# Kernel tuning notes

Measured on AMD Instinct MI355X. Metric: run time of the kernel, lower is better.

## Reference

```python
import jax, jax.numpy as jnp
import numpy as np
from jax import lax

# ---- module config (init_kwargs) ----
B, CIN, COUT, H, W, K = 16, 32, 32, 256, 256, 3
FEATURE_BITS = 8
INPUT_ZP = 3
OUTPUT_ZP = -5
INPUT_SCALE = 0.02
OUTPUT_SCALE = 0.05
STRIDE = (1, 1)
PAD_H, PAD_W = 1, 1
DILATION = (1, 1)
GROUPS = 1
QMIN, QMAX = -(2 ** (FEATURE_BITS - 1)), 2 ** (FEATURE_BITS - 1) - 1  # -128, 127


def float_to_fixed_point(scale, bitwidth):
    # Represent scale (in (0,1)) as int_scale * 2^-frac_bits with int_scale <= 2^(b-1)-1.
    # Pick the largest frac_bits s.t. round(scale * 2^frac_bits) fits -> max precision.
    qmax = jnp.float32(2 ** (bitwidth - 1) - 1)
    frac_bits = jnp.floor(jnp.log2(qmax / scale)).astype(jnp.int32)
    int_scale = jnp.round(scale * jnp.exp2(frac_bits.astype(jnp.float32))).astype(jnp.int32)
    return int_scale, frac_bits


def setup_inputs() -> dict:
    key = jax.random.key(0)
    k0, k1, k2, k3 = jax.random.split(key, 4)
    x = jax.random.randint(k0, (B, CIN, H, W), -128, 128, dtype=jnp.int32).astype(jnp.int8)
    qweight = jax.random.randint(k1, (COUT, CIN, K, K), -128, 128, dtype=jnp.int32).astype(jnp.int8)
    qbias = jax.random.randint(k2, (COUT,), -1000, 1000, dtype=jnp.int32)
    weight_scale = jax.random.uniform(k3, (COUT,), jnp.float32, 1e-3, 1e-2)
    return {"x": x, "qweight": qweight, "qbias": qbias, "weight_scale": weight_scale}


def reference(x, qweight, qbias, weight_scale):
    # F.pad(qinput, (pw,pw,ph,ph), 'constant', input_zero_point) -> pad W and H dims
    xp = jnp.pad(x, ((0, 0), (0, 0), (PAD_H, PAD_H), (PAD_W, PAD_W)),
                 mode="constant", constant_values=INPUT_ZP)
    # int32 conv (no bias), VALID since input was pre-padded
    out = lax.conv_general_dilated(
        xp.astype(jnp.int32), qweight.astype(jnp.int32),
        window_strides=STRIDE, padding="VALID", rhs_dilation=DILATION,
        dimension_numbers=("NCHW", "OIHW", "NCHW"), feature_group_count=GROUPS)
    # shifted bias: qbias - sum(qweight) * input_zero_point  (per out channel)
    shifted_qbias = qbias - qweight.astype(jnp.int32).sum((1, 2, 3)) * INPUT_ZP
    out = out + shifted_qbias[None, :, None, None]
    # fixed-point requant: (out * int_scale) >> frac_bits, per channel
    folded_scale = (INPUT_SCALE * weight_scale / OUTPUT_SCALE).astype(jnp.float32)
    int_scale, frac_bits = float_to_fixed_point(folded_scale, FEATURE_BITS)
    out = jnp.right_shift(out * int_scale[None, :, None, None],
                          frac_bits[None, :, None, None])  # arithmetic shift on int32
    out = out + OUTPUT_ZP
    out = jnp.clip(out, QMIN, QMAX).astype(jnp.int8)
    return out
```

## Files before the change

kernel.cpp:

```cpp
#include <hip/hip_runtime.h>

#define B_   16
#define CIN  32
#define COUT 32
#define H_   256
#define W_   256
#define IN_ZP  3
#define OUT_ZP (-5)
#define HW (H_ * W_)
#define TH 8
#define TW 64
#define SW 72
#define SH 10

#define XPH 258
#define XPW 264
#define XPQ 66
#define PLANE_W (XPH * XPW)
#define XP_WORDS (B_ * 8 * PLANE_W)
#define WS_TAB 2400
#define WS_NEED ((size_t)(WS_TAB + XP_WORDS) * 4)
#define NQ (B_ * 8 * XPH * XPQ)
#define PACK_BLOCKS 2176


using i32x4  = __attribute__((ext_vector_type(4))) int;
using i32x16 = __attribute__((ext_vector_type(16))) int;


__global__ __launch_bounds__(256) void qconv_pack(const int* __restrict__ x,
                                                  const int* __restrict__ qw,
                                                  const int* __restrict__ qb,
                                                  const float* __restrict__ wscale,
                                                  int* __restrict__ ws) {
    const int bid = blockIdx.x;
    const int tid = threadIdx.x;
    if (bid < 32) {
        __shared__ int red[4];
        const int co = bid;
        const int* wco = qw + co * (CIN * 9);
        int s = 0;
        for (int i = tid; i < CIN * 9; i += 256) s += wco[i];
        for (int off = 32; off; off >>= 1) s += __shfl_down(s, off, 64);
        if ((tid & 63) == 0) red[tid >> 6] = s;

        if (tid < 72) {
            int gidx = co * 72 + tid;
            int g    = gidx & 3;
            int lane = (gidx >> 2) & 63;
            int t    = gidx >> 8;
            int wco2 = lane & 31;
            int ci0  = 16 * (lane >> 5) + 4 * g;
            const int* base = qw + wco2 * (CIN * 9);
            int b0 = base[(ci0 + 0) * 9 + t] & 0xff;
            int b1 = base[(ci0 + 1) * 9 + t] & 0xff;
            int b2 = base[(ci0 + 2) * 9 + t] & 0xff;
            int b3 = base[(ci0 + 3) * 9 + t] & 0xff;
            ws[gidx] = b0 | (b1 << 8) | (b2 << 16) | (b3 << 24);
        }
        __syncthreads();
        if (tid == 0) {
            int wsum = red[0] + red[1] + red[2] + red[3];
            ws[2304 + co] = qb[co] - wsum * IN_ZP;
            float fs = (0.02f * wscale[co]) / 0.05f;
            float fb = floorf(log2f(127.0f / fs));
            int isc = (int)rintf(fs * exp2f(fb));
            ws[2336 + co] = isc | (((int)fb) << 16);
        }
        return;
    }
    int* __restrict__ xp = ws + WS_TAB;
    const int T = (PACK_BLOCKS) * 256;
    for (int q = (bid - 32) * 256 + tid; q < NQ; q += T) {
        int b   = q / (8 * XPH * XPQ);
        int r1  = q - b * (8 * XPH * XPQ);
        int cig = r1 / (XPH * XPQ);
        int r2  = r1 - cig * (XPH * XPQ);
        int ph  = r2 / XPQ;
        int cq  = r2 - ph * XPQ;
        int gh  = ph - 1;
        int gw0 = cq * 4 - 4;
        int ghc = min(H_ - 1, max(0, gh));
        int gwc = min(W_ - 4, max(0, gw0));
        const int* p = x + (b * CIN + cig * 4) * HW + ghc * W_ + gwc;
        i32x4 v0 = *(const i32x4*)(p);
        i32x4 v1 = *(const i32x4*)(p + HW);
        i32x4 v2 = *(const i32x4*)(p + 2 * HW);
        i32x4 v3 = *(const i32x4*)(p + 3 * HW);
        bool vh = (unsigned)gh < (unsigned)H_;
        i32x4 pk;
#pragma unroll
        for (int j = 0; j < 4; ++j) {
            int t = (v0[j] & 0xff) | ((v1[j] & 0xff) << 8) |
                    ((v2[j] & 0xff) << 16) | (v3[j] << 24);
            bool ok = vh && ((unsigned)(gw0 + j) < (unsigned)W_);
            pk[j] = ok ? t : 0x03030303;
        }
        *(i32x4*)(xp + 4 * q) = pk;
    }
}

#define SMEM(cig_, r_, c_) sl[((cig_) * SH + (r_)) * SW + (c_)]
__global__ __launch_bounds__(256) void qconv_fused(const int* __restrict__ ws,
                                                   int* __restrict__ out) {
    __shared__ __align__(16) int sl[6144];
    __shared__ __align__(16) int cons[64];

    const int d  = blockIdx.x + 4 * blockIdx.y + 128 * blockIdx.z;
    const int w  = ((d & 7) << 8) | (d >> 3);
    const int tx = w & 3;
    const int ty = (w >> 2) & 31;
    const int tb = w >> 7;

    const int wt = tx * TW;
    const int ht = ty * TH;
    const int tid = threadIdx.x;
    const int lane = tid & 63, wv = tid >> 6;
    const int* __restrict__ xp = ws + WS_TAB;

    if (tid < 64) cons[tid] = ws[2304 + tid];

    const int rowbase = (tb * 8) * XPH + ht;
#pragma unroll
    for (int k = 0; k < 6; ++k) {
        int idx = 256 * k + 64 * wv + lane;
        idx = min(idx, 1439);
        int cig = idx / 180;
        int rem = idx - cig * 180;
        const int* src = xp + (rowbase + cig * XPH + rem / 18) * XPW
                            + wt + 4 * (rem - (rem / 18) * 18);
        __builtin_amdgcn_global_load_lds(
            (const __attribute__((address_space(1))) void*)src,
            (__attribute__((address_space(3))) void*)(sl + 4 * (256 * k + 64 * wv)),
            16, 0, 0);
    }

    i32x4 wfrag[9];
    const i32x4* wsv = (const i32x4*)ws;
#pragma unroll
    for (int t = 0; t < 9; ++t) wfrag[t] = wsv[t * 64 + lane];

    __syncthreads();

    const int hh  = lane >> 5;
    const int pix = lane & 31;

#pragma unroll
    for (int i = 0; i < 4; ++i) {
        const int mt = wv * 4 + i;
        const int r0 = mt >> 1, chunk = mt & 1;
        i32x16 acc;
#pragma unroll
        for (int r = 0; r < 16; ++r) acc[r] = 0;
#pragma unroll
        for (int t = 0; t < 9; ++t) {
            const int dh = t / 3, dw = t % 3;
            const int rr = r0 + dh;
            const int c  = chunk * 32 + pix + dw + 3;
            i32x4 a;
#pragma unroll
            for (int g = 0; g < 4; ++g) a[g] = SMEM(4 * hh + g, rr, c);
            acc = __builtin_amdgcn_mfma_i32_32x32x32_i8(wfrag[t], a, acc, 0, 0, 0);
        }
        int* op = out + (tb * COUT) * HW + (ht + r0) * W_ + wt + chunk * 32 + pix;
#pragma unroll
        for (int rg = 0; rg < 4; ++rg) {
            const int cb = 4 * hh + 8 * rg;
            i32x4 sb4 = *(const i32x4*)&cons[cb];
            i32x4 qf4 = *(const i32x4*)&cons[32 + cb];
#pragma unroll
            for (int j = 0; j < 4; ++j) {
                int q = qf4[j];
                int v = acc[rg * 4 + j] + sb4[j];
                v = (int)((unsigned)v * (unsigned)(q & 0xffff)) >> (q >> 16);
                v += OUT_ZP;
                v = min(127, max(-128, v));
                op[(cb + j) * HW] = v;
            }
        }
    }
}
#undef SMEM

__global__ void qconv_prep_fb(const int* __restrict__ qw, const int* __restrict__ qb,
                              const float* __restrict__ wscale, int* __restrict__ ws) {
    const int co  = blockIdx.x;
    const int tid = threadIdx.x;
    __shared__ int red[4];
    const int* wco = qw + co * (CIN * 9);
    int s = 0;
    for (int i = tid; i < CIN * 9; i += 256) s += wco[i];
    for (int off = 32; off; off >>= 1) s += __shfl_down(s, off, 64);
    if ((tid & 63) == 0) red[tid >> 6] = s;
    if (tid < 72) {
        int gidx = blockIdx.x * 72 + tid;
        int g    = gidx & 3;
        int lane = (gidx >> 2) & 63;
        int t    = gidx >> 8;
        int wco2 = lane & 31;
        int ci0  = 16 * (lane >> 5) + 4 * g;
        const int* base = qw + wco2 * (CIN * 9);
        int b0 = base[(ci0 + 0) * 9 + t] & 0xff;
        int b1 = base[(ci0 + 1) * 9 + t] & 0xff;
        int b2 = base[(ci0 + 2) * 9 + t] & 0xff;
        int b3 = base[(ci0 + 3) * 9 + t] & 0xff;
        ws[gidx] = b0 | (b1 << 8) | (b2 << 16) | (b3 << 24);
    }
    __syncthreads();
    if (tid == 0) {
        int wsum = red[0] + red[1] + red[2] + red[3];
        ws[2304 + co] = qb[co] - wsum * IN_ZP;
        float fs = (0.02f * wscale[co]) / 0.05f;
        float fb = floorf(log2f(127.0f / fs));
        int isc = (int)rintf(fs * exp2f(fb));
        ws[2336 + co] = isc | (((int)fb) << 16);
    }
}

__device__ __forceinline__ void stage_item(int idx, int ht, int wt,
                                           const int* __restrict__ xb,
                                           int (*smem)[SH][SW]) {
    int cig = idx / 180;
    int rem = idx - cig * 180;
    int r   = rem / 18;
    int c4  = rem - r * 18;
    int gh  = ht - 1 + r;
    int gw0 = wt - 4 + c4 * 4;
    int ghc = min(H_ - 1, max(0, gh));
    int gwc = min(W_ - 4, max(0, gw0));
    const int* p = xb + (cig * 4) * HW + ghc * W_ + gwc;
    i32x4 v0 = *(const i32x4*)(p);
    i32x4 v1 = *(const i32x4*)(p + HW);
    i32x4 v2 = *(const i32x4*)(p + 2 * HW);
    i32x4 v3 = *(const i32x4*)(p + 3 * HW);
    bool vh = (unsigned)gh < (unsigned)H_;
    i32x4 pk;
#pragma unroll
    for (int j = 0; j < 4; ++j) {
        int t = (v0[j] & 0xff) | ((v1[j] & 0xff) << 8) |
                ((v2[j] & 0xff) << 16) | (v3[j] << 24);
        bool ok = vh && ((unsigned)(gw0 + j) < (unsigned)W_);
        pk[j] = ok ? t : 0x03030303;
    }
    *(i32x4*)&smem[cig][r][c4 * 4] = pk;
}

__global__ __launch_bounds__(256) void qconv_fused_fb(const int* __restrict__ x,
                                                      const int* __restrict__ ws,
                                                      int* __restrict__ out) {
    __shared__ int smem[8][SH][SW];
    __shared__ __align__(16) int cons[64];
    const int d  = blockIdx.x + 4 * blockIdx.y + 128 * blockIdx.z;
    const int w  = ((d & 7) << 8) | (d >> 3);
    const int tx = w & 3;
    const int ty = (w >> 2) & 31;
    const int tb = w >> 7;
    const int wt = tx * TW;
    const int ht = ty * TH;
    const int tid = threadIdx.x;
    const int* xb = x + tb * (CIN * HW);
    if (tid < 64) cons[tid] = ws[2304 + tid];
    stage_item(tid,        ht, wt, xb, smem);
    stage_item(tid + 256,  ht, wt, xb, smem);
    stage_item(tid + 512,  ht, wt, xb, smem);
    stage_item(tid + 768,  ht, wt, xb, smem);
    stage_item(tid + 1024, ht, wt, xb, smem);
    if (tid < 160) stage_item(tid + 1280, ht, wt, xb, smem);
    __syncthreads();
    const int lane = tid & 63, wv = tid >> 6;
    const int hh  = lane >> 5;
    const int pix = lane & 31;
    i32x4 wfrag[9];
    const i32x4* wsv = (const i32x4*)ws;
#pragma unroll
    for (int t = 0; t < 9; ++t) wfrag[t] = wsv[t * 64 + lane];
#pragma unroll
    for (int i = 0; i < 4; ++i) {
        const int mt = wv * 4 + i;
        const int r0 = mt >> 1, chunk = mt & 1;
        i32x16 acc;
#pragma unroll
        for (int r = 0; r < 16; ++r) acc[r] = 0;
#pragma unroll
        for (int t = 0; t < 9; ++t) {
            const int dh = t / 3, dw = t % 3;
            const int rr = r0 + dh;
            const int c  = chunk * 32 + pix + dw + 3;
            i32x4 a;
#pragma unroll
            for (int g = 0; g < 4; ++g) a[g] = smem[4 * hh + g][rr][c];
            acc = __builtin_amdgcn_mfma_i32_32x32x32_i8(wfrag[t], a, acc, 0, 0, 0);
        }
        int* op = out + (tb * COUT) * HW + (ht + r0) * W_ + wt + chunk * 32 + pix;
#pragma unroll
        for (int rg = 0; rg < 4; ++rg) {
            const int cb = 4 * hh + 8 * rg;
            i32x4 sb4 = *(const i32x4*)&cons[cb];
            i32x4 qf4 = *(const i32x4*)&cons[32 + cb];
#pragma unroll
            for (int j = 0; j < 4; ++j) {
                int q = qf4[j];
                int v = acc[rg * 4 + j] + sb4[j];
                v = (int)((unsigned)v * (unsigned)(q & 0xffff)) >> (q >> 16);
                v += OUT_ZP;
                v = min(127, max(-128, v));
                op[(cb + j) * HW] = v;
            }
        }
    }
}

extern "C" void kernel_launch(void* const* d_in, const int* in_sizes, int n_in,
                              void* d_out, int out_size, void* d_ws, size_t ws_size,
                              hipStream_t stream) {
    const int*   x   = (const int*)d_in[0];
    const int*   qw  = (const int*)d_in[1];
    const int*   qb  = (const int*)d_in[2];
    const float* wsc = (const float*)d_in[3];
    int* ws  = (int*)d_ws;
    int* out = (int*)d_out;
    dim3 grid(W_ / TW, H_ / TH, B_);

    if (ws_size >= WS_NEED) {
        qconv_pack<<<32 + PACK_BLOCKS, 256, 0, stream>>>(x, qw, qb, wsc, ws);
        qconv_fused<<<grid, 256, 0, stream>>>(ws, out);
    } else {
        qconv_prep_fb<<<32, 256, 0, stream>>>(qw, qb, wsc, ws);
        qconv_fused_fb<<<grid, 256, 0, stream>>>(x, ws, out);
    }
}
```

Baseline: 251.1 us.

## Read packed input directly from global memory instead of LDS staging

Removes the shared-memory tile and its global_load_lds staging, so each lane loads the MFMA A operands straight from the packed padded input in global memory, relying on L1/L2 for reuse across the nine taps. The tile loop is no longer unrolled and output stores become nontemporal. This drops the LDS round trip and its latency, but every tap now issues scalar global loads, which adds memory traffic and exposes latency that is no longer hidden behind a single barrier.

```diff
diff --git a/kernel.cpp b/kernel.cpp
--- a/kernel.cpp
+++ b/kernel.cpp
@@ -100,10 +100,8 @@
     }
 }
 
-#define SMEM(cig_, r_, c_) sl[((cig_) * SH + (r_)) * SW + (c_)]
 __global__ __launch_bounds__(256) void qconv_fused(const int* __restrict__ ws,
                                                    int* __restrict__ out) {
-    __shared__ __align__(16) int sl[6144];
     __shared__ __align__(16) int cons[64];
 
     const int d  = blockIdx.x + 4 * blockIdx.y + 128 * blockIdx.z;
@@ -116,24 +114,11 @@
     const int ht = ty * TH;
     const int tid = threadIdx.x;
     const int lane = tid & 63, wv = tid >> 6;
+    const int hh  = lane >> 5;
+    const int pix = lane & 31;
     const int* __restrict__ xp = ws + WS_TAB;
 
     if (tid < 64) cons[tid] = ws[2304 + tid];
-
-    const int rowbase = (tb * 8) * XPH + ht;
-#pragma unroll
-    for (int k = 0; k < 6; ++k) {
-        int idx = 256 * k + 64 * wv + lane;
-        idx = min(idx, 1439);
-        int cig = idx / 180;
-        int rem = idx - cig * 180;
-        const int* src = xp + (rowbase + cig * XPH + rem / 18) * XPW
-                            + wt + 4 * (rem - (rem / 18) * 18);
-        __builtin_amdgcn_global_load_lds(
-            (const __attribute__((address_space(1))) void*)src,
-            (__attribute__((address_space(3))) void*)(sl + 4 * (256 * k + 64 * wv)),
-            16, 0, 0);
-    }
 
     i32x4 wfrag[9];
     const i32x4* wsv = (const i32x4*)ws;
@@ -142,25 +127,28 @@
 
     __syncthreads();
 
-    const int hh  = lane >> 5;
-    const int pix = lane & 31;
-
-#pragma unroll
+    const int rowbase = (tb * 8) * XPH + ht;
+    const int* xbase = xp + rowbase * XPW + wt + pix + 3;
+
+#pragma unroll 1
     for (int i = 0; i < 4; ++i) {
         const int mt = wv * 4 + i;
         const int r0 = mt >> 1, chunk = mt & 1;
+        const int* xt = xbase + (hh * 4) * PLANE_W + r0 * XPW + chunk * 32;
         i32x16 acc;
 #pragma unroll
         for (int r = 0; r < 16; ++r) acc[r] = 0;
 #pragma unroll
-        for (int t = 0; t < 9; ++t) {
-            const int dh = t / 3, dw = t % 3;
-            const int rr = r0 + dh;
-            const int c  = chunk * 32 + pix + dw + 3;
-            i32x4 a;
-#pragma unroll
-            for (int g = 0; g < 4; ++g) a[g] = SMEM(4 * hh + g, rr, c);
-            acc = __builtin_amdgcn_mfma_i32_32x32x32_i8(wfrag[t], a, acc, 0, 0, 0);
+        for (int dh = 0; dh < 3; ++dh) {
+#pragma unroll
+            for (int dw = 0; dw < 3; ++dw) {
+                i32x4 a;
+#pragma unroll
+                for (int g = 0; g < 4; ++g)
+                    a[g] = xt[g * PLANE_W + dh * XPW + dw];
+                acc = __builtin_amdgcn_mfma_i32_32x32x32_i8(
+                          wfrag[dh * 3 + dw], a, acc, 0, 0, 0);
+            }
         }
         int* op = out + (tb * COUT) * HW + (ht + r0) * W_ + wt + chunk * 32 + pix;
 #pragma unroll
@@ -175,12 +163,11 @@
                 v = (int)((unsigned)v * (unsigned)(q & 0xffff)) >> (q >> 16);
                 v += OUT_ZP;
                 v = min(127, max(-128, v));
-                op[(cb + j) * HW] = v;
+                __builtin_nontemporal_store(v, op + (cb + j) * HW);
             }
         }
     }
 }
-#undef SMEM
 
 __global__ void qconv_prep_fb(const int* __restrict__ qw, const int* __restrict__ qb,
                               const float* __restrict__ wscale, int* __restrict__ ws) {
```

Result: no change. 248.0 us (-1.2%).
